# Performance work log

Hardware: AMD Instinct MI355X
Metric: run time of the kernel (lower is better)

Reference implementation:

```python
import jax, jax.numpy as jnp
import numpy as np

UFOLDS = 12
EPS = 1e-08


def _synapse_act(v, mu, sigma, W):
    # v: [B, P]; mu, sigma, W: [P, U] -> activation [B, P, U]
    g = jax.nn.sigmoid(sigma * (v[:, :, None] - mu))
    return W * g


def setup_inputs() -> dict:
    key = jax.random.key(0)
    ks = jax.random.split(key, 13)
    B, IN, U = 2048, 128, 256
    inputs = jax.random.normal(ks[0], (B, IN), dtype=jnp.float32)
    state = jax.random.normal(ks[1], (B, U), dtype=jnp.float32)
    # sensory synapse params (input_size, num_units)
    sensory_mu = jax.random.uniform(ks[2], (IN, U), minval=0.3, maxval=0.8)
    sensory_sigma = jax.random.uniform(ks[3], (IN, U), minval=3.0, maxval=8.0)
    sensory_W = jax.random.uniform(ks[4], (IN, U), minval=0.01, maxval=1.0)
    sensory_erev = jnp.sign(jax.random.normal(ks[5], (IN, U))).astype(jnp.float32)
    # recurrent synapse params (num_units, num_units)
    mu = jax.random.uniform(ks[6], (U, U), minval=0.3, maxval=0.8)
    sigma = jax.random.uniform(ks[7], (U, U), minval=3.0, maxval=8.0)
    W = jax.random.uniform(ks[8], (U, U), minval=0.01, maxval=1.0)
    erev = jnp.sign(jax.random.normal(ks[9], (U, U))).astype(jnp.float32)
    # leak / membrane params (num_units,)
    vleak = jax.random.uniform(ks[10], (U,), minval=-0.2, maxval=0.2)
    gleak = jnp.ones((U,), dtype=jnp.float32)          # gleak_init_min == gleak_init_max == 1
    cm_t = jnp.full((U,), 0.5, dtype=jnp.float32)      # cm_init_min == cm_init_max == 0.5
    return dict(inputs=inputs, state=state,
                sensory_mu=sensory_mu, sensory_sigma=sensory_sigma,
                sensory_W=sensory_W, sensory_erev=sensory_erev,
                mu=mu, sigma=sigma, W=W, erev=erev,
                vleak=vleak, gleak=gleak, cm_t=cm_t)


def reference(inputs, state, sensory_mu, sensory_sigma, sensory_W, sensory_erev,
              mu, sigma, W, erev, vleak, gleak, cm_t):
    # sensory path computed once, outside the fold loop
    s_act = _synapse_act(inputs, sensory_mu, sensory_sigma, sensory_W)  # [B, IN, U]
    w_den_sensory = jnp.sum(s_act, axis=1)                              # [B, U]
    w_num_sensory = jnp.sum(s_act * sensory_erev, axis=1)               # [B, U]

    gl_vl = gleak * vleak  # [U]

    def fold(v_pre, _):
        act = _synapse_act(v_pre, mu, sigma, W)           # [B, U, U]
        w_red = jnp.sum(act, axis=1)                       # [B, U]
        w_num = jnp.sum(act * erev, axis=1) + w_num_sensory
        numerator = cm_t * v_pre + gl_vl + w_num
        denominator = cm_t + gleak + w_red + w_den_sensory
        return numerator / (denominator + EPS), None

    v, _ = jax.lax.scan(fold, state, None, length=UFOLDS)
    return v
```

## Files before the change

kernel.cpp:

```cpp
#include <hip/hip_runtime.h>

#define NFOLDS 12
#define EPS 1e-8f
#define BATCH 2048
#define IN_DIM 128
#define UNITS 256
#define RB 4
#define LOG2E 1.44269504088896340736f

#if __has_builtin(__builtin_amdgcn_exp2f)
#define EXP2F(x) __builtin_amdgcn_exp2f(x)
#else
#define EXP2F(x) exp2f(x)
#endif

#if __has_builtin(__builtin_amdgcn_rcpf)
#define RCPF(x) __builtin_amdgcn_rcpf(x)
#else
#define RCPF(x) (1.0f / (x))
#endif

__global__ void prep_kernel(const float* __restrict__ mu,
                            const float* __restrict__ sigma,
                            const float* __restrict__ W,
                            const float* __restrict__ erev,
                            float4* __restrict__ out, int n) {
    int i = blockIdx.x * blockDim.x + threadIdx.x;
    if (i < n) {
        float A = sigma[i] * LOG2E;
        float w = W[i];
        out[i] = make_float4(-A, A * mu[i], w, w * erev[i]);
    }
}

__device__ __forceinline__ void syn4(const float4 p0, const float4 p1,
                                     const float4 p2, const float4 p3,
                                     const float4 v4, float& red, float& num) {
    {
        float t = fmaf(p0.x, v4.x, p0.y);
        float g = RCPF(1.0f + EXP2F(t));
        red = fmaf(p0.z, g, red);
        num = fmaf(p0.w, g, num);
    }
    {
        float t = fmaf(p1.x, v4.y, p1.y);
        float g = RCPF(1.0f + EXP2F(t));
        red = fmaf(p1.z, g, red);
        num = fmaf(p1.w, g, num);
    }
    {
        float t = fmaf(p2.x, v4.z, p2.y);
        float g = RCPF(1.0f + EXP2F(t));
        red = fmaf(p2.z, g, red);
        num = fmaf(p2.w, g, num);
    }
    {
        float t = fmaf(p3.x, v4.w, p3.y);
        float g = RCPF(1.0f + EXP2F(t));
        red = fmaf(p3.z, g, red);
        num = fmaf(p3.w, g, num);
    }
}

__global__ __launch_bounds__(512, 4) void ltc_kernel(
    const float4* __restrict__ rp,
    const float4* __restrict__ sp,
    const float* __restrict__ inputs,
    const float* __restrict__ state,
    const float* __restrict__ vleak,
    const float* __restrict__ gleak,
    const float* __restrict__ cm_t,
    float* __restrict__ out)
{
    const int tid = threadIdx.x;
    const int u = tid & (UNITS - 1);
    const int h = tid >> 8;
    const int b0 = blockIdx.x * RB;

    __shared__ __align__(16) float v_sh[RB][UNITS];
    __shared__ __align__(16) float in_sh[RB][IN_DIM];
    __shared__ float nb_sh[RB][UNITS];
    __shared__ float db_sh[RB][UNITS];
    __shared__ float cm_sh[UNITS];
    __shared__ float pred[2][RB][UNITS];
    __shared__ float pnum[2][RB][UNITS];

    if (h == 0) {
        #pragma unroll
        for (int rb = 0; rb < RB; ++rb)
            v_sh[rb][u] = state[(b0 + rb) * UNITS + u];
        cm_sh[u] = cm_t[u];
    } else {
        #pragma unroll
        for (int k = u; k < RB * IN_DIM; k += UNITS) {
            int rb = k >> 7;
            int i  = k & (IN_DIM - 1);
            in_sh[rb][i] = inputs[(b0 + rb) * IN_DIM + i];
        }
    }
    __syncthreads();

    {
        float sden[RB] = {0.f, 0.f, 0.f, 0.f};
        float snum[RB] = {0.f, 0.f, 0.f, 0.f};
        const int ibase = h * (IN_DIM / 2);
        for (int ic = 0; ic < IN_DIM / 2; ic += 4) {
            const int i = ibase + ic;
            float4 p0 = sp[(i + 0) * UNITS + u];
            float4 p1 = sp[(i + 1) * UNITS + u];
            float4 p2 = sp[(i + 2) * UNITS + u];
            float4 p3 = sp[(i + 3) * UNITS + u];
            #pragma unroll
            for (int rb = 0; rb < RB; ++rb) {
                float4 x4 = *reinterpret_cast<const float4*>(&in_sh[rb][i]);
                syn4(p0, p1, p2, p3, x4, sden[rb], snum[rb]);
            }
        }
        #pragma unroll
        for (int rb = 0; rb < RB; ++rb) {
            pred[h][rb][u] = sden[rb];
            pnum[h][rb][u] = snum[rb];
        }
    }
    __syncthreads();

    #pragma unroll
    for (int k = 0; k < 2; ++k) {
        const int rb = h + 2 * k;
        float gl = gleak[u];
        float sd = pred[0][rb][u] + pred[1][rb][u];
        float sn = pnum[0][rb][u] + pnum[1][rb][u];
        db_sh[rb][u] = cm_sh[u] + gl + sd + EPS;
        nb_sh[rb][u] = fmaf(gl, vleak[u], sn);
    }
    __syncthreads();

    for (int f = 0; f < NFOLDS; ++f) {
        float wred[RB] = {0.f, 0.f, 0.f, 0.f};
        float wnum[RB] = {0.f, 0.f, 0.f, 0.f};
        const int jbase = h * (UNITS / 2);
        for (int jc = 0; jc < UNITS / 2; jc += 4) {
            const int j = jbase + jc;
            float4 p0 = rp[(j + 0) * UNITS + u];
            float4 p1 = rp[(j + 1) * UNITS + u];
            float4 p2 = rp[(j + 2) * UNITS + u];
            float4 p3 = rp[(j + 3) * UNITS + u];
            #pragma unroll
            for (int rb = 0; rb < RB; ++rb) {
                float4 v4 = *reinterpret_cast<const float4*>(&v_sh[rb][j]);
                syn4(p0, p1, p2, p3, v4, wred[rb], wnum[rb]);
            }
        }
        #pragma unroll
        for (int rb = 0; rb < RB; ++rb) {
            pred[h][rb][u] = wred[rb];
            pnum[h][rb][u] = wnum[rb];
        }
        __syncthreads();

        #pragma unroll
        for (int k = 0; k < 2; ++k) {
            const int rb = h + 2 * k;
            float wr = pred[0][rb][u] + pred[1][rb][u];
            float wn = pnum[0][rb][u] + pnum[1][rb][u];
            float vp = v_sh[rb][u];
            float num = fmaf(cm_sh[u], vp, nb_sh[rb][u]) + wn;
            float den = db_sh[rb][u] + wr;
            float vn = num / den;
            v_sh[rb][u] = vn;
            if (f == NFOLDS - 1)
                out[(b0 + rb) * UNITS + u] = vn;
        }
        __syncthreads();
    }
}

extern "C" void kernel_launch(void* const* d_in, const int* in_sizes, int n_in,
                              void* d_out, int out_size, void* d_ws, size_t ws_size,
                              hipStream_t stream) {
    const float* inputs       = (const float*)d_in[0];
    const float* state        = (const float*)d_in[1];
    const float* sensory_mu   = (const float*)d_in[2];
    const float* sensory_sig  = (const float*)d_in[3];
    const float* sensory_W    = (const float*)d_in[4];
    const float* sensory_erev = (const float*)d_in[5];
    const float* mu           = (const float*)d_in[6];
    const float* sigma        = (const float*)d_in[7];
    const float* W            = (const float*)d_in[8];
    const float* erev         = (const float*)d_in[9];
    const float* vleak        = (const float*)d_in[10];
    const float* gleak        = (const float*)d_in[11];
    const float* cm_t         = (const float*)d_in[12];
    float* out = (float*)d_out;

    float4* rp = (float4*)d_ws;
    float4* sp = rp + UNITS * UNITS;

    int n_rec = UNITS * UNITS;
    int n_sen = IN_DIM * UNITS;
    prep_kernel<<<(n_rec + 255) / 256, 256, 0, stream>>>(mu, sigma, W, erev, rp, n_rec);
    prep_kernel<<<(n_sen + 255) / 256, 256, 0, stream>>>(sensory_mu, sensory_sig,
                                                         sensory_W, sensory_erev, sp, n_sen);

    ltc_kernel<<<BATCH / RB, 512, 0, stream>>>(rp, sp, inputs, state,
                                               vleak, gleak, cm_t, out);
}
```

Before: 385.9 us.

## Compute synapse sigmoids in packed fp16 with polynomial exp2 and Newton reciprocal

```diff
diff --git a/kernel.cpp b/kernel.cpp
--- a/kernel.cpp
+++ b/kernel.cpp
@@ -1,4 +1,5 @@
 #include <hip/hip_runtime.h>
+#include <hip/hip_fp16.h>
 
 #define NFOLDS 12
 #define EPS 1e-8f
@@ -8,63 +9,102 @@
 #define RB 4
 #define LOG2E 1.44269504088896340736f
 
-#if __has_builtin(__builtin_amdgcn_exp2f)
-#define EXP2F(x) __builtin_amdgcn_exp2f(x)
-#else
-#define EXP2F(x) exp2f(x)
-#endif
-
 #if __has_builtin(__builtin_amdgcn_rcpf)
 #define RCPF(x) __builtin_amdgcn_rcpf(x)
 #else
 #define RCPF(x) (1.0f / (x))
 #endif
 
-__global__ void prep_kernel(const float* __restrict__ mu,
-                            const float* __restrict__ sigma,
-                            const float* __restrict__ W,
-                            const float* __restrict__ erev,
-                            float4* __restrict__ out, int n) {
+typedef _Float16 v2h __attribute__((ext_vector_type(2)));
+
+__device__ __forceinline__ unsigned pk_fma_h(unsigned a, unsigned b, unsigned c) {
+    unsigned d;
+    asm("v_pk_fma_f16 %0, %1, %2, %3" : "=v"(d) : "v"(a), "v"(b), "v"(c));
+    return d;
+}
+__device__ __forceinline__ unsigned pk_add_h(unsigned a, unsigned b) {
+    unsigned d;
+    asm("v_pk_add_f16 %0, %1, %2" : "=v"(d) : "v"(a), "v"(b));
+    return d;
+}
+__device__ __forceinline__ unsigned pk_max_h(unsigned a, unsigned b) {
+    unsigned d;
+    asm("v_pk_max_f16 %0, %1, %2" : "=v"(d) : "v"(a), "v"(b));
+    return d;
+}
+__device__ __forceinline__ unsigned pk_min_h(unsigned a, unsigned b) {
+    unsigned d;
+    asm("v_pk_min_f16 %0, %1, %2" : "=v"(d) : "v"(a), "v"(b));
+    return d;
+}
+__device__ __forceinline__ unsigned pksub16(unsigned a, unsigned b) {
+    unsigned d;
+    asm("v_pk_sub_u16 %0, %1, %2" : "=v"(d) : "v"(a), "v"(b));
+    return d;
+}
+__device__ __forceinline__ unsigned pkshl16(unsigned sh, unsigned a) {
+    unsigned d;
+    asm("v_pk_lshlrev_b16 %0, %1, %2" : "=v"(d) : "v"(sh), "v"(a));
+    return d;
+}
+
+struct KC {
+    unsigned c1536, negc1536, none, one, nc1, nc2, nc3, hi12, lo12;
+    unsigned k497, sh10, rmagic;
+};
+
+__device__ __forceinline__ void chain(const uint4 q, unsigned v2u, const KC& K,
+                                      float& red, float& num) {
+    unsigned t = pk_fma_h(q.x, v2u, q.y);
+    t = pk_max_h(t, K.lo12);
+    t = pk_min_h(t, K.hi12);
+    unsigned z = pk_add_h(t, K.c1536);
+    unsigned n = pk_add_h(z, K.negc1536);
+    unsigned f = pk_fma_h(n, K.none, t);
+    unsigned p = pk_fma_h(K.nc3, f, K.nc2);
+    p = pk_fma_h(p, f, K.nc1);
+    p = pk_fma_h(p, f, K.none);
+    unsigned s = pkshl16(K.sh10, pksub16(z, K.k497));
+    unsigned nA = pk_fma_h(p, s, K.none);
+    unsigned r = pksub16(K.rmagic, nA);
+    unsigned e = pk_fma_h(nA, r, K.one);
+    r = pk_fma_h(r, e, r);
+    e = pk_fma_h(nA, r, K.one);
+    r = pk_fma_h(r, e, r);
+    v2h rr = __builtin_bit_cast(v2h, r);
+    red = __builtin_amdgcn_fdot2(__builtin_bit_cast(v2h, q.z), rr, red, false);
+    num = __builtin_amdgcn_fdot2(__builtin_bit_cast(v2h, q.w), rr, num, false);
+}
+
+__global__ void prep_h2_kernel(const float* __restrict__ mu,
+                               const float* __restrict__ sigma,
+                               const float* __restrict__ W,
+                               const float* __restrict__ erev,
+                               uint4* __restrict__ out, int n) {
     int i = blockIdx.x * blockDim.x + threadIdx.x;
     if (i < n) {
-        float A = sigma[i] * LOG2E;
-        float w = W[i];
-        out[i] = make_float4(-A, A * mu[i], w, w * erev[i]);
-    }
-}
-
-__device__ __forceinline__ void syn4(const float4 p0, const float4 p1,
-                                     const float4 p2, const float4 p3,
-                                     const float4 v4, float& red, float& num) {
-    {
-        float t = fmaf(p0.x, v4.x, p0.y);
-        float g = RCPF(1.0f + EXP2F(t));
-        red = fmaf(p0.z, g, red);
-        num = fmaf(p0.w, g, num);
-    }
-    {
-        float t = fmaf(p1.x, v4.y, p1.y);
-        float g = RCPF(1.0f + EXP2F(t));
-        red = fmaf(p1.z, g, red);
-        num = fmaf(p1.w, g, num);
-    }
-    {
-        float t = fmaf(p2.x, v4.z, p2.y);
-        float g = RCPF(1.0f + EXP2F(t));
-        red = fmaf(p2.z, g, red);
-        num = fmaf(p2.w, g, num);
-    }
-    {
-        float t = fmaf(p3.x, v4.w, p3.y);
-        float g = RCPF(1.0f + EXP2F(t));
-        red = fmaf(p3.z, g, red);
-        num = fmaf(p3.w, g, num);
+        int p = i >> 8;
+        int u = i & (UNITS - 1);
+        int i0 = (2 * p) * UNITS + u;
+        int i1 = i0 + UNITS;
+        float A0 = sigma[i0] * LOG2E, A1 = sigma[i1] * LOG2E;
+        __half2 a2, b2, w2, e2;
+        a2.x = __float2half(-A0);              a2.y = __float2half(-A1);
+        b2.x = __float2half(A0 * mu[i0]);      b2.y = __float2half(A1 * mu[i1]);
+        w2.x = __float2half(W[i0]);            w2.y = __float2half(W[i1]);
+        e2.x = __float2half(W[i0] * erev[i0]); e2.y = __float2half(W[i1] * erev[i1]);
+        uint4 o;
+        o.x = __builtin_bit_cast(unsigned, a2);
+        o.y = __builtin_bit_cast(unsigned, b2);
+        o.z = __builtin_bit_cast(unsigned, w2);
+        o.w = __builtin_bit_cast(unsigned, e2);
+        out[i] = o;
     }
 }
 
 __global__ __launch_bounds__(512, 4) void ltc_kernel(
-    const float4* __restrict__ rp,
-    const float4* __restrict__ sp,
+    const uint4* __restrict__ rq,
+    const uint4* __restrict__ sq,
     const float* __restrict__ inputs,
     const float* __restrict__ state,
     const float* __restrict__ vleak,
@@ -77,8 +117,22 @@
     const int h = tid >> 8;
     const int b0 = blockIdx.x * RB;
 
-    __shared__ __align__(16) float v_sh[RB][UNITS];
-    __shared__ __align__(16) float in_sh[RB][IN_DIM];
+    KC K;
+    K.c1536    = __builtin_bit_cast(unsigned, __float2half2_rn(1536.0f));
+    K.negc1536 = __builtin_bit_cast(unsigned, __float2half2_rn(-1536.0f));
+    K.none     = __builtin_bit_cast(unsigned, __float2half2_rn(-1.0f));
+    K.one      = __builtin_bit_cast(unsigned, __float2half2_rn(1.0f));
+    K.nc1      = __builtin_bit_cast(unsigned, __float2half2_rn(-0.6931472f));
+    K.nc2      = __builtin_bit_cast(unsigned, __float2half2_rn(-0.2401397f));
+    K.nc3      = __builtin_bit_cast(unsigned, __float2half2_rn(-0.0558282f));
+    K.hi12     = __builtin_bit_cast(unsigned, __float2half2_rn(12.0f));
+    K.lo12     = __builtin_bit_cast(unsigned, __float2half2_rn(-12.0f));
+    K.k497  = 0x01F101F1u;
+    K.sh10  = 0x000A000Au;
+    K.rmagic = 0xF7B6F7B6u;
+
+    __shared__ unsigned vp_sh[RB][UNITS / 2];
+    __shared__ unsigned in_sh[RB][IN_DIM / 2];
     __shared__ float nb_sh[RB][UNITS];
     __shared__ float db_sh[RB][UNITS];
     __shared__ float cm_sh[UNITS];
@@ -87,33 +141,36 @@
 
     if (h == 0) {
         #pragma unroll
-        for (int rb = 0; rb < RB; ++rb)
-            v_sh[rb][u] = state[(b0 + rb) * UNITS + u];
+        for (int k = u; k < RB * (UNITS / 2); k += UNITS) {
+            int rb = k >> 7, p = k & 127;
+            const float* src = state + (b0 + rb) * UNITS + 2 * p;
+            __half2 hh; hh.x = __float2half(src[0]); hh.y = __float2half(src[1]);
+            vp_sh[rb][p] = __builtin_bit_cast(unsigned, hh);
+        }
         cm_sh[u] = cm_t[u];
     } else {
-        #pragma unroll
-        for (int k = u; k < RB * IN_DIM; k += UNITS) {
-            int rb = k >> 7;
-            int i  = k & (IN_DIM - 1);
-            in_sh[rb][i] = inputs[(b0 + rb) * IN_DIM + i];
-        }
-    }
+        int rb = u >> 6, p = u & 63;
+        const float* src = inputs + (b0 + rb) * IN_DIM + 2 * p;
+        __half2 hh; hh.x = __float2half(src[0]); hh.y = __float2half(src[1]);
+        in_sh[rb][p] = __builtin_bit_cast(unsigned, hh);
+    }
+    float vfull[2];
+    #pragma unroll
+    for (int k = 0; k < 2; ++k)
+        vfull[k] = state[(b0 + h + 2 * k) * UNITS + u];
     __syncthreads();
 
     {
         float sden[RB] = {0.f, 0.f, 0.f, 0.f};
         float snum[RB] = {0.f, 0.f, 0.f, 0.f};
-        const int ibase = h * (IN_DIM / 2);
-        for (int ic = 0; ic < IN_DIM / 2; ic += 4) {
-            const int i = ibase + ic;
-            float4 p0 = sp[(i + 0) * UNITS + u];
-            float4 p1 = sp[(i + 1) * UNITS + u];
-            float4 p2 = sp[(i + 2) * UNITS + u];
-            float4 p3 = sp[(i + 3) * UNITS + u];
+        for (int pr = h * 32; pr < h * 32 + 32; pr += 2) {
+            uint4 q0 = sq[(pr + 0) * UNITS + u];
+            uint4 q1 = sq[(pr + 1) * UNITS + u];
             #pragma unroll
             for (int rb = 0; rb < RB; ++rb) {
-                float4 x4 = *reinterpret_cast<const float4*>(&in_sh[rb][i]);
-                syn4(p0, p1, p2, p3, x4, sden[rb], snum[rb]);
+                uint2 vv = *reinterpret_cast<const uint2*>(&in_sh[rb][pr]);
+                chain(q0, vv.x, K, sden[rb], snum[rb]);
+                chain(q1, vv.y, K, sden[rb], snum[rb]);
             }
         }
         #pragma unroll
@@ -138,17 +195,14 @@
     for (int f = 0; f < NFOLDS; ++f) {
         float wred[RB] = {0.f, 0.f, 0.f, 0.f};
         float wnum[RB] = {0.f, 0.f, 0.f, 0.f};
-        const int jbase = h * (UNITS / 2);
-        for (int jc = 0; jc < UNITS / 2; jc += 4) {
-            const int j = jbase + jc;
-            float4 p0 = rp[(j + 0) * UNITS + u];
-            float4 p1 = rp[(j + 1) * UNITS + u];
-            float4 p2 = rp[(j + 2) * UNITS + u];
-            float4 p3 = rp[(j + 3) * UNITS + u];
+        for (int pr = h * 64; pr < h * 64 + 64; pr += 2) {
+            uint4 q0 = rq[(pr + 0) * UNITS + u];
+            uint4 q1 = rq[(pr + 1) * UNITS + u];
             #pragma unroll
             for (int rb = 0; rb < RB; ++rb) {
-                float4 v4 = *reinterpret_cast<const float4*>(&v_sh[rb][j]);
-                syn4(p0, p1, p2, p3, v4, wred[rb], wnum[rb]);
+                uint2 vv = *reinterpret_cast<const uint2*>(&vp_sh[rb][pr]);
+                chain(q0, vv.x, K, wred[rb], wnum[rb]);
+                chain(q1, vv.y, K, wred[rb], wnum[rb]);
             }
         }
         #pragma unroll
@@ -158,18 +212,26 @@
         }
         __syncthreads();
 
+        float vn[2];
         #pragma unroll
         for (int k = 0; k < 2; ++k) {
             const int rb = h + 2 * k;
             float wr = pred[0][rb][u] + pred[1][rb][u];
             float wn = pnum[0][rb][u] + pnum[1][rb][u];
-            float vp = v_sh[rb][u];
-            float num = fmaf(cm_sh[u], vp, nb_sh[rb][u]) + wn;
+            float num = fmaf(cm_sh[u], vfull[k], nb_sh[rb][u]) + wn;
             float den = db_sh[rb][u] + wr;
-            float vn = num / den;
-            v_sh[rb][u] = vn;
+            vn[k] = num * RCPF(den);
+            vfull[k] = vn[k];
             if (f == NFOLDS - 1)
-                out[(b0 + rb) * UNITS + u] = vn;
+                out[(b0 + rb) * UNITS + u] = vn[k];
+        }
+        float o0 = __shfl_xor(vn[0], 1);
+        float o1 = __shfl_xor(vn[1], 1);
+        if (!(u & 1)) {
+            __half2 p0; p0.x = __float2half(vn[0]); p0.y = __float2half(o0);
+            __half2 p1; p1.x = __float2half(vn[1]); p1.y = __float2half(o1);
+            vp_sh[h][u >> 1]     = __builtin_bit_cast(unsigned, p0);
+            vp_sh[h + 2][u >> 1] = __builtin_bit_cast(unsigned, p1);
         }
         __syncthreads();
     }
@@ -193,15 +255,16 @@
     const float* cm_t         = (const float*)d_in[12];
     float* out = (float*)d_out;
 
-    float4* rp = (float4*)d_ws;
-    float4* sp = rp + UNITS * UNITS;
-
-    int n_rec = UNITS * UNITS;
-    int n_sen = IN_DIM * UNITS;
-    prep_kernel<<<(n_rec + 255) / 256, 256, 0, stream>>>(mu, sigma, W, erev, rp, n_rec);
-    prep_kernel<<<(n_sen + 255) / 256, 256, 0, stream>>>(sensory_mu, sensory_sig,
-                                                         sensory_W, sensory_erev, sp, n_sen);
-
-    ltc_kernel<<<BATCH / RB, 512, 0, stream>>>(rp, sp, inputs, state,
+    uint4* rq = (uint4*)d_ws;
+    uint4* sq = rq + (UNITS / 2) * UNITS;
+
+    int n_rec = (UNITS / 2) * UNITS;
+    int n_sen = (IN_DIM / 2) * UNITS;
+    prep_h2_kernel<<<(n_rec + 255) / 256, 256, 0, stream>>>(
+        mu, sigma, W, erev, rq, n_rec);
+    prep_h2_kernel<<<(n_sen + 255) / 256, 256, 0, stream>>>(
+        sensory_mu, sensory_sig, sensory_W, sensory_erev, sq, n_sen);
+
+    ltc_kernel<<<BATCH / RB, 512, 0, stream>>>(rq, sq, inputs, state,
                                                vleak, gleak, cm_t, out);
 }
```

New measurement: 500.6 us. +29.7%, slower.
